# Performance work log

Hardware: AMD Instinct MI355X
Metric: run time of the kernel (lower is better)

The kernel has to match this reference:

```python
import jax, jax.numpy as jnp
import numpy as np

THRESH = 0.5      # jaccard_thresh
NEGPOS = 3        # neg:pos ratio for hard negative mining
VAR0, VAR1 = 0.1, 0.2  # SSD encoding variances


def point_form(boxes):
    # center-size [P,4] -> (xmin,ymin,xmax,ymax)
    return jnp.concatenate([boxes[:, :2] - boxes[:, 2:] / 2,
                            boxes[:, :2] + boxes[:, 2:] / 2], axis=1)


def jaccard(box_a, box_b):
    # box_a [O,4], box_b [P,4] point-form -> IoU [O,P]
    lt = jnp.maximum(box_a[:, None, :2], box_b[None, :, :2])
    rb = jnp.minimum(box_a[:, None, 2:], box_b[None, :, 2:])
    wh = jnp.clip(rb - lt, 0.0)
    inter = wh[..., 0] * wh[..., 1]
    area_a = ((box_a[:, 2] - box_a[:, 0]) * (box_a[:, 3] - box_a[:, 1]))[:, None]
    area_b = ((box_b[:, 2] - box_b[:, 0]) * (box_b[:, 3] - box_b[:, 1]))[None, :]
    return inter / (area_a + area_b - inter)


def encode(matched, priors):
    # matched point-form [P,4], priors center-size [P,4]
    g_cxcy = ((matched[:, :2] + matched[:, 2:]) / 2 - priors[:, :2]) / (VAR0 * priors[:, 2:])
    g_wh = jnp.log((matched[:, 2:] - matched[:, :2]) / priors[:, 2:]) / VAR1
    return jnp.concatenate([g_cxcy, g_wh], axis=1)


def match_one(truths, labels, priors):
    # truths [O,4] point-form, labels [O] int, priors [P,4] center-size
    O = truths.shape[0]
    ov = jaccard(truths, point_form(priors))          # [O,P]
    best_prior_idx = jnp.argmax(ov, axis=1)           # [O]
    best_truth_ov = jnp.max(ov, axis=0)               # [P]
    best_truth_idx = jnp.argmax(ov, axis=0)           # [P]
    # ensure each gt matches its best prior
    best_truth_ov = best_truth_ov.at[best_prior_idx].set(2.0)
    best_truth_idx = best_truth_idx.at[best_prior_idx].set(jnp.arange(O))
    matches = truths[best_truth_idx]                  # [P,4]
    conf = jnp.where(best_truth_ov < THRESH, 0, labels[best_truth_idx] + 1)
    return encode(matches, priors), conf


def setup_inputs() -> dict:
    key = jax.random.key(0)
    ks = jax.random.split(key, 6)
    B, P, C, O = 32, 24656, 81, 16
    predictions = jax.random.normal(ks[0], (B, P, 4 + C), dtype=jnp.float32)
    # priors: center-size, valid w/h
    pc = jax.random.uniform(ks[1], (P, 2), minval=0.05, maxval=0.95)
    pwh = jax.random.uniform(ks[2], (P, 2), minval=0.02, maxval=0.3)
    priors = jnp.concatenate([pc, pwh], axis=1).astype(jnp.float32)
    # ground-truth boxes in point form, guaranteed positive extent
    tc = jax.random.uniform(ks[3], (B, O, 2), minval=0.2, maxval=0.8)
    twh = jax.random.uniform(ks[4], (B, O, 2), minval=0.05, maxval=0.3)
    targets_boxes = jnp.concatenate([tc - twh / 2, tc + twh / 2], axis=-1).astype(jnp.float32)
    targets_labels = jax.random.randint(ks[5], (B, O), 0, C - 1, dtype=jnp.int32)
    return {"predictions": predictions, "targets_boxes": targets_boxes,
            "targets_labels": targets_labels, "priors": priors}


def reference(predictions, targets_boxes, targets_labels, priors):
    loc_data = predictions[..., :4]        # [B,P,4]
    conf_data = predictions[..., 4:]       # [B,P,C]
    B, P = loc_data.shape[:2]
    C = conf_data.shape[2]

    loc_t, conf_t = jax.vmap(match_one, in_axes=(0, 0, None))(
        targets_boxes, targets_labels, priors)   # [B,P,4], [B,P]

    pos = conf_t > 0                                   # [B,P]
    # smooth L1 on positives, sum reduction
    d = loc_data - loc_t
    ad = jnp.abs(d)
    sl1 = jnp.where(ad < 1.0, 0.5 * d * d, ad - 0.5)
    loss_l = jnp.sum(sl1 * pos[..., None].astype(sl1.dtype))

    # per-anchor cross entropy
    logp = jax.nn.log_softmax(conf_data, axis=-1)
    lbl = jnp.clip(conf_t, 0, C - 1)
    ce = -jnp.take_along_axis(logp, lbl[..., None], axis=-1)[..., 0]  # [B,P]

    # hard negative mining: rank negatives by loss (positives zeroed)
    loss_rank = jnp.where(pos, 0.0, ce)
    loss_idx = jnp.argsort(-loss_rank, axis=1)
    idx_rank = jnp.argsort(loss_idx, axis=1)
    num_pos = jnp.sum(pos, axis=1, keepdims=True)          # [B,1]
    num_neg = jnp.minimum(num_pos * NEGPOS, P)
    neg = idx_rank < num_neg

    sel = (pos | neg).astype(ce.dtype)
    loss_c = jnp.sum(ce * sel)

    N = jnp.sum(num_pos).astype(loss_l.dtype)
    return loss_l / N, loss_c / N
```

## Files before the change

### kernel.cpp

```cpp
#include <hip/hip_runtime.h>
#include <math.h>

#define NB 32
#define NP 24656
#define NO 16
#define NC 81
#define ND 85
#define THRESH_F 0.5f
#define NEGPOS_I 3
#define VAR0_F 0.1f
#define VAR1_F 0.2f
#define NEG_HUGE -1e30f

#define BPCNT (NB * NP)
#define MBLK2 25
#define CHB32 771
#define SPB2 56
#define CB32 11264

typedef unsigned long long u64;

__global__ __launch_bounds__(256) void k_match(
    const float* __restrict__ tboxes, const float* __restrict__ priors,
    float2* __restrict__ bt2, u64* __restrict__ mcand,
    int* __restrict__ npos, float* __restrict__ accB, int* __restrict__ done) {
    const int b = blockIdx.y, bx = blockIdx.x, tid = threadIdx.x;
    const int lane = tid & 63, wv = tid >> 6;
    __shared__ float tb[NO * 4];
    __shared__ u64 wkey[4][NO];
    if (bx == 0 && b == 0) {
        if (tid < NB) npos[tid] = 0;
        if (tid < 2 * NB) accB[tid] = 0.f;
        if (tid == 0) *done = 0;
    }
    if (tid < NO * 4) tb[tid] = tboxes[b * NO * 4 + tid];
    __syncthreads();

    const int p0 = bx * 1024 + tid * 4;
    float pl[4], pt[4], prr[4], pbm[4], pa[4];
    bool pv[4];
#pragma unroll
    for (int j = 0; j < 4; ++j) {
        const int p = p0 + j;
        pv[j] = (p < NP);
        const float4 q = pv[j] ? ((const float4*)priors)[p]
                               : make_float4(0.f, 0.f, 1.f, 1.f);
        pl[j] = q.x - q.z * 0.5f; pt[j] = q.y - q.w * 0.5f;
        prr[j] = q.x + q.z * 0.5f; pbm[j] = q.y + q.w * 0.5f;
        pa[j] = (prr[j] - pl[j]) * (pbm[j] - pt[j]);
    }
    float bestv[4] = {-1.f, -1.f, -1.f, -1.f};
    int besti[4] = {0, 0, 0, 0};
    for (int o = 0; o < NO; ++o) {
        const float al = tb[o * 4], at = tb[o * 4 + 1];
        const float ar = tb[o * 4 + 2], ab = tb[o * 4 + 3];
        const float aarea = (ar - al) * (ab - at);
        u64 kmax = 0ull;
#pragma unroll
        for (int j = 0; j < 4; ++j) {
            float iw = fminf(ar, prr[j]) - fmaxf(al, pl[j]); iw = fmaxf(iw, 0.f);
            float ih = fminf(ab, pbm[j]) - fmaxf(at, pt[j]); ih = fmaxf(ih, 0.f);
            const float inter = iw * ih;
            const float iou = inter / (aarea + pa[j] - inter);
            if (pv[j]) {
                if (iou > bestv[j]) { bestv[j] = iou; besti[j] = o; }
                const u64 key = ((u64)__float_as_uint(iou) << 32) |
                                (u64)(0xFFFFFFFFu - (unsigned)(p0 + j));
                kmax = (key > kmax) ? key : kmax;
            }
        }
        for (int d = 1; d < 64; d <<= 1) {
            const u64 other = __shfl_xor(kmax, d, 64);
            kmax = (other > kmax) ? other : kmax;
        }
        if (lane == 0) wkey[wv][o] = kmax;
    }
#pragma unroll
    for (int j = 0; j < 4; ++j)
        if (pv[j])
            bt2[(size_t)b * NP + p0 + j] =
                make_float2(bestv[j], __int_as_float(besti[j]));
    __syncthreads();
    if (tid < NO) {
        u64 k0 = wkey[0][tid];
        k0 = (wkey[1][tid] > k0) ? wkey[1][tid] : k0;
        k0 = (wkey[2][tid] > k0) ? wkey[2][tid] : k0;
        k0 = (wkey[3][tid] > k0) ? wkey[3][tid] : k0;
        mcand[((size_t)(b * NO + tid)) * MBLK2 + bx] = k0;
    }
}

__device__ __forceinline__ void stage_load(float4* vreg,
                                           const char* __restrict__ gpred,
                                           int b, int r0, int lane) {
    const size_t off = ((size_t)b * NP + r0) * 340ull;
    const char* g = gpred + off;
    const bool unsafe = (b == NB - 1) && (r0 + 34 > NP);
    if (!unsafe) {
#pragma unroll
        for (int k = 0; k < 11; ++k)
            vreg[k] = *(const float4*)(g + k * 1024 + lane * 16);
    } else {
        const int nf4 = (NP - r0) * ND / 4;
        const float4* gs = (const float4*)g;
#pragma unroll
        for (int k = 0; k < 11; ++k) {
            const int idx = k * 64 + lane;
            vreg[k] = (idx < nf4) ? gs[idx]
                                  : make_float4(0.f, 0.f, 0.f, 0.f);
        }
    }
}

__device__ __forceinline__ void stage_write(char* buf, const float4* vreg,
                                            int lane) {
#pragma unroll
    for (int k = 0; k < 11; ++k)
        *(float4*)(buf + k * 1024 + lane * 16) = vreg[k];
}

__global__ __launch_bounds__(64) void k_main(
    const float* __restrict__ pred, const float* __restrict__ tboxes,
    const int* __restrict__ tlabels, const float* __restrict__ priors,
    const float2* __restrict__ bt2, const u64* __restrict__ mcand,
    float* __restrict__ lr, int* __restrict__ npos, float* __restrict__ accB) {
    __shared__ char smem[2][CB32];

    const int b = blockIdx.y;
    const int span = blockIdx.x;
    const int lane = threadIdx.x;
    const size_t bbase = (size_t)b * NP;
    const char* gpred = (const char*)pred;

    char* cur = smem[0];
    char* nxt = smem[1];

    const int rho = lane >> 1;
    const int h = lane & 1;
    const int c0 = rho & 3;
    const int Ab = 16 * (21 * rho + (rho >> 2));
    const int sbase = h ? 11 : 1;

    u64 pbk = 0ull;
    if (lane < NO) {
        const u64* c = mcand + (size_t)(b * NO + lane) * MBLK2;
        for (int i = 0; i < MBLK2; ++i) {
            const u64 v = c[i];
            pbk = (v > pbk) ? v : pbk;
        }
    }
    int p16[NO];
#pragma unroll
    for (int j = 0; j < NO; ++j) {
        const u64 kj = __shfl(pbk, j, 64);
        p16[j] = (int)(0xFFFFFFFFu - (unsigned)(kj & 0xFFFFFFFFull));
    }

    float my_ll = 0.f, my_ce = 0.f;
    int my_np = 0;

    int chunk = span;
    int next_chunk = chunk + SPB2;
    {
        float4 vreg[11];
        stage_load(vreg, gpred, b, chunk * 32, lane);
        stage_write(cur, vreg, lane);
    }

    while (chunk < CHB32) {
        float4 vreg[11];
        const bool have_next = (next_chunk < CHB32);
        if (have_next)
            stage_load(vreg, gpred, b, next_chunk * 32, lane);

        const int r0 = chunk * 32;
        const int nrows = min(32, NP - r0);

        float4 v[11];
#pragma unroll
        for (int k = 0; k < 11; ++k)
            v[k] = *(const float4*)(cur + Ab + 16 * (sbase + k));

        float vals[44];
#pragma unroll
        for (int k = 0; k < 11; ++k) {
            const float xs[4] = {v[k].x, v[k].y, v[k].z, v[k].w};
#pragma unroll
            for (int t = 0; t < 4; ++t) {
                bool ok;
                if (k == 0)
                    ok = h ? false : (t >= c0);
                else if (k == 10)
                    ok = h ? (t <= c0) : true;
                else
                    ok = true;
                vals[4 * k + t] = ok ? xs[t] : NEG_HUGE;
            }
        }
        float mA = vals[0], mB = vals[1];
#pragma unroll
        for (int j = 2; j < 44; j += 2) {
            mA = fmaxf(mA, vals[j]);
            mB = fmaxf(mB, vals[j + 1]);
        }
        float m = fmaxf(mA, mB);
        m = fmaxf(m, __shfl_xor(m, 1, 64));

        float sA = 0.f, sB = 0.f;
#pragma unroll
        for (int j = 0; j < 44; j += 2) {
            sA += __expf(vals[j] - m);
            sB += __expf(vals[j + 1] - m);
        }
        float ssum = sA + sB;
        ssum += __shfl_xor(ssum, 1, 64);
        const float lse = m + __logf(ssum);

        if (h == 0 && rho < nrows) {
            const float bg = (c0 == 0) ? v[0].x : (c0 == 1) ? v[0].y
                           : (c0 == 2) ? v[0].z : v[0].w;
            const int p = r0 + rho;
            const float2 bt = bt2[bbase + p];
            int o_f = -1;
#pragma unroll
            for (int j = 0; j < NO; ++j)
                if (p == p16[j]) o_f = j;
            const bool forced = (o_f >= 0);
            const bool pos = forced || (bt.x >= THRESH_F);
            const int o = forced ? o_f : __float_as_int(bt.y);
            lr[bbase + p] = pos ? 0.f : (lse - bg);
            if (pos) {
                my_np += 1;
                const float* rowp = (const float*)(cur + 340 * rho);
                const int lbl = tlabels[b * NO + o] + 1;
                my_ce += lse - rowp[4 + lbl];
                const float4 pq = *((const float4*)priors + p);
                const float tx0 = tboxes[(b * NO + o) * 4 + 0];
                const float ty0 = tboxes[(b * NO + o) * 4 + 1];
                const float tx1 = tboxes[(b * NO + o) * 4 + 2];
                const float ty1 = tboxes[(b * NO + o) * 4 + 3];
                const float g0 = ((tx0 + tx1) * 0.5f - pq.x) / (VAR0_F * pq.z);
                const float g1 = ((ty0 + ty1) * 0.5f - pq.y) / (VAR0_F * pq.w);
                const float g2 = __logf((tx1 - tx0) / pq.z) / VAR1_F;
                const float g3 = __logf((ty1 - ty0) / pq.w) / VAR1_F;
                float dd, ad;
                dd = rowp[0] - g0; ad = fabsf(dd); my_ll += (ad < 1.f) ? 0.5f * dd * dd : (ad - 0.5f);
                dd = rowp[1] - g1; ad = fabsf(dd); my_ll += (ad < 1.f) ? 0.5f * dd * dd : (ad - 0.5f);
                dd = rowp[2] - g2; ad = fabsf(dd); my_ll += (ad < 1.f) ? 0.5f * dd * dd : (ad - 0.5f);
                dd = rowp[3] - g3; ad = fabsf(dd); my_ll += (ad < 1.f) ? 0.5f * dd * dd : (ad - 0.5f);
            }
        }

        if (have_next)
            stage_write(nxt, vreg, lane);

        chunk = next_chunk;
        next_chunk += SPB2;
        char* tmp = cur; cur = nxt; nxt = tmp;
    }

    for (int d2 = 1; d2 < 64; d2 <<= 1) {
        my_ll += __shfl_xor(my_ll, d2, 64);
        my_ce += __shfl_xor(my_ce, d2, 64);
        my_np += __shfl_xor(my_np, d2, 64);
    }
    if (lane == 0) {
        if (my_ll != 0.f) atomicAdd(&accB[b * 2 + 0], my_ll);
        if (my_ce != 0.f) atomicAdd(&accB[b * 2 + 1], my_ce);
        if (my_np) atomicAdd(&npos[b], my_np);
    }
}

__global__ __launch_bounds__(1024) void k_select(
    const float* __restrict__ lrk, const int* __restrict__ npos,
    float* __restrict__ accB, int* __restrict__ done, float* __restrict__ out) {
    const int b = blockIdx.x;
    const float* row = lrk + (size_t)b * NP;
    const float4* row4 = (const float4*)row;
    const int tid = threadIdx.x;
    const int lane = tid & 63;
    const int wid = tid >> 6;
    const int sub = lane & 15;

    __shared__ unsigned hist16[2048][16];
    __shared__ unsigned chist[2048];
    __shared__ int sh_bucket, sh_knew;
    __shared__ float wsum[16];
    __shared__ int wcnt[16];

    const int K0 = min(npos[b] * NEGPOS_I, NP);
    int k = K0;
    unsigned prefix = 0;

    const int shifts[3] = {21, 10, 0};
    const unsigned masks[3] = {0u, 0xFFE00000u, 0xFFFFFC00u};

    for (int pass = 0; pass < 3; ++pass) {
        const int shift = shifts[pass];
        const unsigned mask_hi = masks[pass];
        {
            unsigned* hflat = (unsigned*)hist16;
            for (int j = tid; j < 2048 * 16; j += 1024) hflat[j] = 0;
        }
        __syncthreads();
        for (int i = tid; i < NP / 4; i += 1024) {
            const float4 v4 = row4[i];
#pragma unroll
            for (int c = 0; c < 4; ++c) {
                const float f = (c == 0) ? v4.x : (c == 1) ? v4.y
                              : (c == 2) ? v4.z : v4.w;
                const unsigned v = __float_as_uint(f);
                if ((v & mask_hi) == (prefix & mask_hi))
                    atomicAdd(&hist16[(v >> shift) & 2047u][sub], 1u);
            }
        }
        __syncthreads();
        for (int j = tid; j < 2048; j += 1024) {
            unsigned t = 0;
#pragma unroll
            for (int s = 0; s < 16; ++s) t += hist16[j][s];
            chist[j] = t;
        }
        __syncthreads();
        if (tid < 64) {
            unsigned g = 0;
            for (int j = 0; j < 32; ++j) g += chist[lane * 32 + j];
            unsigned T = g;
            for (int d = 1; d < 64; d <<= 1) {
                const unsigned t = __shfl_down(T, d, 64);
                if (lane + d < 64) T += t;
            }
            const unsigned E = T - g;
            const bool hit = (E < (unsigned)k) && ((unsigned)k <= T);
            const unsigned long long msk = __ballot(hit);
            const int wl = __ffsll(msk) - 1;
            if (lane == wl) {
                unsigned cum = E;
                int bsel = lane * 32, kn = k;
                for (int j = 31; j >= 0; --j) {
                    const unsigned c = chist[lane * 32 + j];
                    if (cum + c >= (unsigned)k) {
                        bsel = lane * 32 + j;
                        kn = k - (int)cum;
                        break;
                    }
                    cum += c;
                }
                sh_bucket = bsel;
                sh_knew = kn;
            }
        }
        __syncthreads();
        prefix |= ((unsigned)sh_bucket) << shift;
        k = sh_knew;
        __syncthreads();
    }
    const float T = __uint_as_float(prefix);

    float msum = 0.f;
    int mcnt = 0;
    for (int i = tid; i < NP / 4; i += 1024) {
        const float4 v4 = row4[i];
#pragma unroll
        for (int c = 0; c < 4; ++c) {
            const float f = (c == 0) ? v4.x : (c == 1) ? v4.y
                          : (c == 2) ? v4.z : v4.w;
            if (__float_as_uint(f) > prefix) { msum += f; mcnt++; }
        }
    }
    for (int s = 32; s > 0; s >>= 1) {
        msum += __shfl_down(msum, s, 64);
        mcnt += __shfl_down(mcnt, s, 64);
    }
    if (lane == 0) { wsum[wid] = msum; wcnt[wid] = mcnt; }
    __syncthreads();
    if (tid == 0) {
        float tot = 0.f;
        int cnt = 0;
        for (int w = 0; w < 16; ++w) { tot += wsum[w]; cnt += wcnt[w]; }
        atomicAdd(&accB[b * 2 + 1], tot + (float)(K0 - cnt) * T);
        __threadfence();
        if (atomicAdd(done, 1) == NB - 1) {
            volatile const float* va = accB;
            volatile const int* vn = npos;
            int n = 0;
            float a0 = 0.f, a1 = 0.f;
            for (int bb = 0; bb < NB; ++bb) {
                n += vn[bb];
                a0 += va[bb * 2 + 0];
                a1 += va[bb * 2 + 1];
            }
            const float N = (float)n;
            out[0] = a0 / N;
            out[1] = a1 / N;
        }
    }
}

extern "C" void kernel_launch(void* const* d_in, const int* in_sizes, int n_in,
                              void* d_out, int out_size, void* d_ws, size_t ws_size,
                              hipStream_t stream) {
    const float* pred   = (const float*)d_in[0];
    const float* tboxes = (const float*)d_in[1];
    const int*   tlabels = (const int*)d_in[2];
    const float* priors = (const float*)d_in[3];
    float* out = (float*)d_out;

    char* w = (char*)d_ws;
    float2* bt2 = (float2*)w;
    float*  lrk = (float*)(w + 8ull * BPCNT);
    u64*    mcand = (u64*)(w + 12ull * BPCNT);
    char*   w2 = w + 12ull * BPCNT + 8ull * NB * NO * MBLK2;
    int*    npos = (int*)w2;
    float*  accB = (float*)(w2 + 4ull * NB);
    int*    done = (int*)(w2 + 4ull * NB + 8ull * NB);

    k_match<<<dim3(MBLK2, NB), dim3(256), 0, stream>>>(
        tboxes, priors, bt2, mcand, npos, accB, done);
    k_main<<<dim3(SPB2, NB), dim3(64), 0, stream>>>(
        pred, tboxes, tlabels, priors, bt2, mcand, lrk, npos, accB);
    k_select<<<dim3(NB), dim3(1024), 0, stream>>>(lrk, npos, accB, done, out);
}
```

Measured before the change: 116.2 us.

## Cache loss row in registers for radix select; reduce match keys via shared memory

The radix-select kernel now loads each batch row's loss values into registers once (7 float4 per thread) and reuses them across the three histogram passes and the final sum, instead of rereading global memory four times. Histogram clearing and summing switch to 128-bit shared accesses. In the match kernel, the per-object wave shuffle reduction of argmax keys is replaced by a two-stage shared-memory max reduction run after the loop. These changes add register pressure in the 1024-thread select kernel and a large shared buffer (NO*256 u64) in the match kernel, which may lower occupancy.

```diff
diff --git a/kernel.cpp b/kernel.cpp
--- a/kernel.cpp
+++ b/kernel.cpp
@@ -25,9 +25,9 @@
     float2* __restrict__ bt2, u64* __restrict__ mcand,
     int* __restrict__ npos, float* __restrict__ accB, int* __restrict__ done) {
     const int b = blockIdx.y, bx = blockIdx.x, tid = threadIdx.x;
-    const int lane = tid & 63, wv = tid >> 6;
     __shared__ float tb[NO * 4];
-    __shared__ u64 wkey[4][NO];
+    __shared__ u64 kbuf[NO][256];
+    __shared__ u64 pbuf[NO][16];
     if (bx == 0 && b == 0) {
         if (tid < NB) npos[tid] = 0;
         if (tid < 2 * NB) accB[tid] = 0.f;
@@ -69,11 +69,7 @@
                 kmax = (key > kmax) ? key : kmax;
             }
         }
-        for (int d = 1; d < 64; d <<= 1) {
-            const u64 other = __shfl_xor(kmax, d, 64);
-            kmax = (other > kmax) ? other : kmax;
-        }
-        if (lane == 0) wkey[wv][o] = kmax;
+        kbuf[o][tid] = kmax;
     }
 #pragma unroll
     for (int j = 0; j < 4; ++j)
@@ -81,12 +77,25 @@
             bt2[(size_t)b * NP + p0 + j] =
                 make_float2(bestv[j], __int_as_float(besti[j]));
     __syncthreads();
+    {
+        const int o = tid >> 4, seg = tid & 15;
+        u64 m = kbuf[o][seg];
+#pragma unroll
+        for (int i = 1; i < 16; ++i) {
+            const u64 v = kbuf[o][i * 16 + seg];
+            m = (v > m) ? v : m;
+        }
+        pbuf[o][seg] = m;
+    }
+    __syncthreads();
     if (tid < NO) {
-        u64 k0 = wkey[0][tid];
-        k0 = (wkey[1][tid] > k0) ? wkey[1][tid] : k0;
-        k0 = (wkey[2][tid] > k0) ? wkey[2][tid] : k0;
-        k0 = (wkey[3][tid] > k0) ? wkey[3][tid] : k0;
-        mcand[((size_t)(b * NO + tid)) * MBLK2 + bx] = k0;
+        u64 m = pbuf[tid][0];
+#pragma unroll
+        for (int i = 1; i < 16; ++i) {
+            const u64 v = pbuf[tid][i];
+            m = (v > m) ? v : m;
+        }
+        mcand[((size_t)(b * NO + tid)) * MBLK2 + bx] = m;
     }
 }
 
@@ -275,8 +284,7 @@
     const float* __restrict__ lrk, const int* __restrict__ npos,
     float* __restrict__ accB, int* __restrict__ done, float* __restrict__ out) {
     const int b = blockIdx.x;
-    const float* row = lrk + (size_t)b * NP;
-    const float4* row4 = (const float4*)row;
+    const float4* row4 = (const float4*)(lrk + (size_t)b * NP);
     const int tid = threadIdx.x;
     const int lane = tid & 63;
     const int wid = tid >> 6;
@@ -288,6 +296,15 @@
     __shared__ float wsum[16];
     __shared__ int wcnt[16];
 
+    float4 cch[7];
+    bool cvz[7];
+#pragma unroll
+    for (int j = 0; j < 7; ++j) {
+        const int i = tid + j * 1024;
+        cvz[j] = (i < NP / 4);
+        cch[j] = cvz[j] ? row4[i] : make_float4(0.f, 0.f, 0.f, 0.f);
+    }
+
     const int K0 = min(npos[b] * NEGPOS_I, NP);
     int k = K0;
     unsigned prefix = 0;
@@ -299,27 +316,31 @@
         const int shift = shifts[pass];
         const unsigned mask_hi = masks[pass];
         {
-            unsigned* hflat = (unsigned*)hist16;
-            for (int j = tid; j < 2048 * 16; j += 1024) hflat[j] = 0;
+            uint4* hz = (uint4*)hist16;
+            for (int j = tid; j < 2048 * 4; j += 1024)
+                hz[j] = make_uint4(0u, 0u, 0u, 0u);
         }
         __syncthreads();
-        for (int i = tid; i < NP / 4; i += 1024) {
-            const float4 v4 = row4[i];
-#pragma unroll
-            for (int c = 0; c < 4; ++c) {
-                const float f = (c == 0) ? v4.x : (c == 1) ? v4.y
-                              : (c == 2) ? v4.z : v4.w;
-                const unsigned v = __float_as_uint(f);
-                if ((v & mask_hi) == (prefix & mask_hi))
-                    atomicAdd(&hist16[(v >> shift) & 2047u][sub], 1u);
+#pragma unroll
+        for (int j = 0; j < 7; ++j) {
+            if (cvz[j]) {
+                const float4 v4 = cch[j];
+#pragma unroll
+                for (int c = 0; c < 4; ++c) {
+                    const float f = (c == 0) ? v4.x : (c == 1) ? v4.y
+                                  : (c == 2) ? v4.z : v4.w;
+                    const unsigned v = __float_as_uint(f);
+                    if ((v & mask_hi) == (prefix & mask_hi))
+                        atomicAdd(&hist16[(v >> shift) & 2047u][sub], 1u);
+                }
             }
         }
         __syncthreads();
         for (int j = tid; j < 2048; j += 1024) {
-            unsigned t = 0;
-#pragma unroll
-            for (int s = 0; s < 16; ++s) t += hist16[j][s];
-            chist[j] = t;
+            const uint4* hp = (const uint4*)&hist16[j][0];
+            const uint4 a = hp[0], b4 = hp[1], c4 = hp[2], d4 = hp[3];
+            chist[j] = a.x + a.y + a.z + a.w + b4.x + b4.y + b4.z + b4.w +
+                       c4.x + c4.y + c4.z + c4.w + d4.x + d4.y + d4.z + d4.w;
         }
         __syncthreads();
         if (tid < 64) {
@@ -359,13 +380,16 @@
 
     float msum = 0.f;
     int mcnt = 0;
-    for (int i = tid; i < NP / 4; i += 1024) {
-        const float4 v4 = row4[i];
-#pragma unroll
-        for (int c = 0; c < 4; ++c) {
-            const float f = (c == 0) ? v4.x : (c == 1) ? v4.y
-                          : (c == 2) ? v4.z : v4.w;
-            if (__float_as_uint(f) > prefix) { msum += f; mcnt++; }
+#pragma unroll
+    for (int j = 0; j < 7; ++j) {
+        if (cvz[j]) {
+            const float4 v4 = cch[j];
+#pragma unroll
+            for (int c = 0; c < 4; ++c) {
+                const float f = (c == 0) ? v4.x : (c == 1) ? v4.y
+                              : (c == 2) ? v4.z : v4.w;
+                if (__float_as_uint(f) > prefix) { msum += f; mcnt++; }
+            }
         }
     }
     for (int s = 32; s > 0; s >>= 1) {
```

Result: faster. 107.8 us (-7.3%).
